# Kernel tuning notes

Hardware: AMD Instinct MI355X
Metric: run time of the kernel (lower is better)

Reference implementation:

```python
import jax, jax.numpy as jnp
import numpy as np
from jax import lax

# ---- Haar (db1) wavelet filters, matching create_wavelet_filter ----
_S2 = float(1.0 / np.sqrt(2.0))
_dec_lo = np.array([_S2, _S2], np.float32)    # pywt dec_lo reversed (symmetric)
_dec_hi = np.array([_S2, -_S2], np.float32)   # pywt dec_hi [-s,s] reversed
_rec_lo = np.array([_S2, _S2], np.float32)    # pywt rec_lo flipped (symmetric)
_rec_hi = np.array([-_S2, _S2], np.float32)   # pywt rec_hi [s,-s] flipped

def _outer(a, b):  # torch: a.unsqueeze(0) * b.unsqueeze(1) -> [i,j] = a[j]*b[i]
    return b[:, None] * a[None, :]

DEC = jnp.asarray(np.stack([_outer(_dec_lo, _dec_lo), _outer(_dec_lo, _dec_hi),
                            _outer(_dec_hi, _dec_lo), _outer(_dec_hi, _dec_hi)]))  # [4,2,2]
REC = jnp.asarray(np.stack([_outer(_rec_lo, _rec_lo), _outer(_rec_lo, _rec_hi),
                            _outer(_rec_hi, _rec_lo), _outer(_rec_hi, _rec_hi)]))  # [4,2,2]

BN_EPS = 1e-5

def mish(x):
    return x * jnp.tanh(jax.nn.softplus(x))

def silu(x):
    return x * jax.nn.sigmoid(x)

def bn(x, g, b):  # eval-mode BatchNorm2d with running_mean=0, running_var=1
    return x * (g / jnp.sqrt(1.0 + BN_EPS))[None, :, None, None] + b[None, :, None, None]

def dwconv(x, w, pad):  # depthwise conv, w: [C,1,k,k]
    return lax.conv_general_dilated(x, w, (1, 1), [(pad, pad), (pad, pad)],
                                    feature_group_count=x.shape[1],
                                    dimension_numbers=('NCHW', 'OIHW', 'NCHW'))

def dyn_dwconv(x, ew, gw):
    # DynamicConv2d (depthwise experts). ew: [E,C,1,k,k], gw: [E,C]
    gates = jax.nn.softmax(x.mean((2, 3)) @ gw.T, axis=-1)  # [B,E]
    k = ew.shape[-1]
    outs = jnp.stack([dwconv(x, ew[e], k // 2) for e in range(ew.shape[0])], 1)  # [B,E,C,H,W]
    return jnp.einsum('be,bechw->bchw', gates, outs)

def local_branch(x, ew, gw, bn1g, bn1b, pw, bn2g, bn2b):
    # DWConv2d_BN_ReLU: dynamic dwconv -> BN -> Mish -> depthwise 1x1 (per-channel scale) -> BN
    y = mish(bn(dyn_dwconv(x, ew, gw), bn1g, bn1b))
    y = y * pw[None, :, None, None]
    return bn(y, bn2g, bn2b)

def sel_scan(u, xw, dtw, dtb, Alog, Dp):
    # u: [B,L,D]; xw: [R+2N,D]; dtw: [D,R]; dtb: [D]; Alog: [D,N]; Dp: [D]
    R = dtw.shape[1]
    N = Alog.shape[1]
    xdbl = jnp.einsum('bld,ed->ble', u, xw)
    dt, Bm, Cm = xdbl[..., :R], xdbl[..., R:R + N], xdbl[..., R + N:]
    delta = jax.nn.softplus(jnp.einsum('blr,dr->bld', dt, dtw) + dtb)  # [B,L,D]
    A = -jnp.exp(Alog)                                                  # [D,N]
    a = jnp.exp(delta[..., None] * A)                                   # [B,L,D,N]
    b = delta[..., None] * Bm[:, :, None, :] * u[..., None]             # [B,L,D,N]
    def comb(c1, c2):
        a1, b1 = c1
        a2, b2 = c2
        return a1 * a2, a2 * b1 + b2
    _, h = lax.associative_scan(comb, (a, b), axis=1)                    # h_t = a_t h_{t-1} + b_t
    return jnp.einsum('bldn,bln->bld', h, Cm) + Dp * u

def ss2d(x, in_w, cw, cb, xpw, dtw, dtb, Alog, Dp, ow):
    # SS2D (d_state=1, k_group=2, channel_first): in_proj -> dwconv+silu -> 2-direction
    # selective scan -> gate with silu(z) -> out_proj.
    B, C, H, W = x.shape
    xz = jnp.einsum('oc,bchw->bohw', in_w, x)
    d = in_w.shape[0] // 2
    xi, z = xz[:, :d], xz[:, d:]
    xc = silu(dwconv(xi, cw, 1) + cb[None, :, None, None])
    u0 = xc.reshape(B, d, H * W).transpose(0, 2, 1)                       # row-major scan
    u1 = xc.transpose(0, 1, 3, 2).reshape(B, d, H * W).transpose(0, 2, 1)  # col-major scan
    y0 = sel_scan(u0, xpw[0], dtw[0], dtb[0], Alog[0], Dp[0])
    y1 = sel_scan(u1, xpw[1], dtw[1], dtb[1], Alog[1], Dp[1])
    y0 = y0.transpose(0, 2, 1).reshape(B, d, H, W)
    y1 = y1.transpose(0, 2, 1).reshape(B, d, W, H).transpose(0, 1, 3, 2)
    y = (y0 + y1) * silu(z)
    return jnp.einsum('oc,bchw->bohw', ow, y)

def mbwt(x, wav_w, wav_b, wav_scale, base_scale,
         ss_in_w, ss_conv_w, ss_conv_b, ss_xproj_w, ss_dt_w, ss_dt_b, ss_A_log, ss_D, ss_out_w):
    # MBWTConv2d, wt_levels=1, H/W even. Haar WT (2x2 stride 2) == block reshape + einsum.
    B, C, H, W = x.shape
    xr = x.reshape(B, C, H // 2, 2, W // 2, 2)
    wt = jnp.einsum('bchpwq,kpq->bckhw', xr, DEC)                  # [B,C,4,h,w]
    tag = wt.reshape(B, 4 * C, H // 2, W // 2)
    tag = dwconv(tag, wav_w, wav_w.shape[-1] // 2) + wav_b[None, :, None, None]
    tag = (tag * wav_scale).reshape(B, C, 4, H // 2, W // 2)
    # inverse Haar WT (conv_transpose 2x2 stride 2, groups=C)
    up = jnp.einsum('bckhw,kpq->bchpwq', tag, REC).reshape(B, C, H, W)
    g = ss2d(x, ss_in_w, ss_conv_w, ss_conv_b, ss_xproj_w, ss_dt_w, ss_dt_b, ss_A_log, ss_D, ss_out_w)
    return base_scale * g + up


def setup_inputs() -> dict:
    key = jax.random.key(0)
    ks = iter(jax.random.split(key, 64))
    B, DIM, H, W = 16, 256, 64, 64
    Cg = Cl = 64
    d = {'x': jax.random.normal(next(ks), (B, DIM, H, W), jnp.float32)}
    for j, k in enumerate((3, 5, 7)):
        p = f'l{j}_'
        d[p + 'ew'] = jax.random.normal(next(ks), (4, Cl, 1, k, k), jnp.float32) * 0.1
        d[p + 'gw'] = jax.random.normal(next(ks), (4, Cl), jnp.float32) * 0.1
        d[p + 'bn1g'] = jnp.ones((Cl,), jnp.float32)
        d[p + 'bn1b'] = jnp.zeros((Cl,), jnp.float32)
        d[p + 'pw'] = jax.random.normal(next(ks), (Cl,), jnp.float32) * 0.2
        d[p + 'bn2g'] = jnp.ones((Cl,), jnp.float32)
        d[p + 'bn2b'] = jnp.zeros((Cl,), jnp.float32)
    d['wav_w'] = jax.random.normal(next(ks), (4 * Cg, 1, 3, 3), jnp.float32) * 0.1
    d['wav_b'] = jnp.zeros((4 * Cg,), jnp.float32)
    d['wav_scale'] = jnp.full((1, 4 * Cg, 1, 1), 0.1, jnp.float32)
    d['base_scale'] = jnp.ones((1, Cg, 1, 1), jnp.float32)
    dm, R, N, K = Cg, 4, 1, 2  # d_inner, dt_rank, d_state, k_group
    d['ss_in_w'] = jax.random.normal(next(ks), (2 * dm, Cg), jnp.float32) * float(1 / np.sqrt(Cg))
    d['ss_conv_w'] = jax.random.normal(next(ks), (dm, 1, 3, 3), jnp.float32) * 0.1
    d['ss_conv_b'] = jnp.zeros((dm,), jnp.float32)
    d['ss_xproj_w'] = jax.random.normal(next(ks), (K, R + 2 * N, dm), jnp.float32) * float(1 / np.sqrt(dm))
    d['ss_dt_w'] = jax.random.normal(next(ks), (K, dm, R), jnp.float32) * float(1 / np.sqrt(R))
    d['ss_dt_b'] = jnp.full((K, dm), -2.0, jnp.float32)
    d['ss_A_log'] = jnp.zeros((K, dm, N), jnp.float32)
    d['ss_D'] = jnp.ones((K, dm), jnp.float32)
    d['ss_out_w'] = jax.random.normal(next(ks), (Cg, dm), jnp.float32) * float(1 / np.sqrt(dm))
    return d


def reference(x,
              l0_ew, l0_gw, l0_bn1g, l0_bn1b, l0_pw, l0_bn2g, l0_bn2b,
              l1_ew, l1_gw, l1_bn1g, l1_bn1b, l1_pw, l1_bn2g, l1_bn2b,
              l2_ew, l2_gw, l2_bn1g, l2_bn1b, l2_pw, l2_bn2g, l2_bn2b,
              wav_w, wav_b, wav_scale, base_scale,
              ss_in_w, ss_conv_w, ss_conv_b, ss_xproj_w, ss_dt_w, ss_dt_b, ss_A_log, ss_D, ss_out_w):
    Cg, Cl = 64, 64
    xg, xl, xi = x[:, :Cg], x[:, Cg:Cg + Cl], x[:, Cg + Cl:]
    yl = (local_branch(xl, l0_ew, l0_gw, l0_bn1g, l0_bn1b, l0_pw, l0_bn2g, l0_bn2b)
          + local_branch(xl, l1_ew, l1_gw, l1_bn1g, l1_bn1b, l1_pw, l1_bn2g, l1_bn2b)
          + local_branch(xl, l2_ew, l2_gw, l2_bn1g, l2_bn1b, l2_pw, l2_bn2g, l2_bn2b))
    yg = mbwt(xg, wav_w, wav_b, wav_scale, base_scale,
              ss_in_w, ss_conv_w, ss_conv_b, ss_xproj_w, ss_dt_w, ss_dt_b, ss_A_log, ss_D, ss_out_w)
    return jnp.concatenate([yg, yl, xi], axis=1)
```

## Files before the change

### kernel.cpp

```cpp
#include <hip/hip_runtime.h>
#include <math.h>

static constexpr int NB   = 16;
static constexpr int DIM  = 256;
static constexpr int CG   = 64;
static constexpr int HH   = 64;
static constexpr int WW   = 64;
static constexpr int HW   = HH * WW;

__device__ __forceinline__ float mish_fast(float x) {
    float t = __expf(fminf(x, 20.f));
    float p = __builtin_fmaf(t, t, t + t);
    return x * p * __builtin_amdgcn_rcpf(p + 2.f);
}
__device__ __forceinline__ float silu_f(float x) {
    return x * __builtin_amdgcn_rcpf(1.f + __expf(-x));
}
__device__ __forceinline__ float softplus_fast(float x) {
    return fmaxf(x, 0.f) + __logf(1.f + __expf(-fabsf(x)));
}

__global__ __launch_bounds__(256) void k_stage1(
    const float* __restrict__ x,
    const float* __restrict__ wav_w, const float* __restrict__ wav_b,
    const float* __restrict__ wav_scale,
    float* __restrict__ up, float* __restrict__ mean,
    const float* __restrict__ in_w,
    float* __restrict__ xi, float* __restrict__ z,
    float* __restrict__ out) {
    __shared__ float smem[4608];
    int bid = blockIdx.x;
    int tid = threadIdx.x;
    int role = bid % 7;

    if (role < 4) {
        int aid = (bid / 7) * 4 + role;
        int c = aid & 63, b = aid >> 6;
        float* wtb = smem;
        float* red = smem + 4352;
        const float* xp = x + ((size_t)b * DIM + c) * HW;

        {
            const float4* lp4 = (const float4*)(x + ((size_t)b * DIM + 64 + c) * HW);
            float s = 0.f;
            for (int i = tid; i < 1024; i += 256) {
                float4 v = lp4[i];
                s += (v.x + v.y) + (v.z + v.w);
            }
            red[tid] = s;
            __syncthreads();
            for (int o = 128; o > 0; o >>= 1) {
                if (tid < o) red[tid] += red[tid + o];
                __syncthreads();
            }
            if (tid == 0) mean[b * 64 + c] = red[0] * (1.f / HW);
        }

#pragma unroll
        for (int it = 0; it < 2; ++it) {
            int p = tid + it * 256;
            int h = p >> 4, w2 = p & 15;
            float4 top = *(const float4*)(xp + (2 * h) * 64 + 4 * w2);
            float4 bot = *(const float4*)(xp + (2 * h + 1) * 64 + 4 * w2);
            float a0 = top.x, b0 = top.y, c0q = bot.x, d0 = bot.y;
            float a1 = top.z, b1 = top.w, c1q = bot.z, d1 = bot.w;
            int base0 = h * 34 + 2 * w2;
            *(float2*)(wtb + 0 * 1088 + base0) =
                make_float2(0.5f * (a0 + b0 + c0q + d0), 0.5f * (a1 + b1 + c1q + d1));
            *(float2*)(wtb + 1 * 1088 + base0) =
                make_float2(0.5f * (a0 + b0 - c0q - d0), 0.5f * (a1 + b1 - c1q - d1));
            *(float2*)(wtb + 2 * 1088 + base0) =
                make_float2(0.5f * (a0 - b0 + c0q - d0), 0.5f * (a1 - b1 + c1q - d1));
            *(float2*)(wtb + 3 * 1088 + base0) =
                make_float2(0.5f * (a0 - b0 - c0q + d0), 0.5f * (a1 - b1 - c1q + d1));
        }
        __syncthreads();

        float wk[4][9], tb[4];
#pragma unroll
        for (int k = 0; k < 4; ++k) {
            int ch = c * 4 + k;
            float sc = wav_scale[ch];
#pragma unroll
            for (int j = 0; j < 9; ++j) wk[k][j] = wav_w[ch * 9 + j] * sc;
            tb[k] = wav_b[ch] * sc;
        }
        float* upp = up + ((size_t)b * CG + c) * HW;
        for (int i = tid; i < 1024; i += 256) {
            int h = i >> 5, w = i & 31;
            float tg[4];
#pragma unroll
            for (int k = 0; k < 4; ++k) {
                float s = tb[k];
#pragma unroll
                for (int dy = -1; dy <= 1; ++dy) {
                    int hh = h + dy;
                    if (hh < 0 || hh >= 32) continue;
#pragma unroll
                    for (int dx = -1; dx <= 1; ++dx) {
                        int wx = w + dx;
                        if (wx < 0 || wx >= 32) continue;
                        s = fmaf(wtb[k * 1088 + hh * 34 + wx], wk[k][(dy + 1) * 3 + (dx + 1)], s);
                    }
                }
                tg[k] = s;
            }
            float u00 = 0.5f * (tg[0] - tg[1] - tg[2] + tg[3]);
            float u01 = 0.5f * (tg[0] - tg[1] + tg[2] - tg[3]);
            float u10 = 0.5f * (tg[0] + tg[1] - tg[2] - tg[3]);
            float u11 = 0.5f * (tg[0] + tg[1] + tg[2] + tg[3]);
            *(float2*)(upp + (2 * h) * 64 + 2 * w)     = make_float2(u00, u01);
            *(float2*)(upp + (2 * h + 1) * 64 + 2 * w) = make_float2(u10, u11);
        }
    } else if (role < 6) {
        int did = (bid / 7) * 2 + (role - 4);
        int h0 = (did & 31) * 2;
        int b  = did >> 5;
        float* xs = smem;
        float* wt = smem + 2048;

        float acc[8][8];
#pragma unroll
        for (int i = 0; i < 8; ++i)
#pragma unroll
            for (int j = 0; j < 8; ++j) acc[i][j] = 0.f;

        int o0 = (tid >> 4) * 8;
        int p0 = (tid & 15) * 8;

        for (int ko = 0; ko < 64; ko += 16) {
            if (ko) __syncthreads();
            {
                int s = tid;
#pragma unroll
                for (int it = 0; it < 2; ++it, s += 256) {
                    int c = s >> 5, p4 = (s & 31) * 4;
                    float4 v = *(const float4*)(x + ((size_t)b * DIM + ko + c) * HW + h0 * 64 + p4);
                    *(float4*)(xs + c * 128 + p4) = v;
                }
            }
            {
                int s = tid;
#pragma unroll
                for (int it = 0; it < 2; ++it, s += 256) {
                    int o = s >> 2, c0 = (s & 3) * 4;
                    float4 v = *(const float4*)(in_w + o * 64 + ko + c0);
#pragma unroll
                    for (int i = 0; i < 4; ++i) {
                        int cc = c0 + i;
                        int osw = o ^ (((cc >> 2) & 3) << 3);
                        wt[cc * 128 + osw] = ((const float*)&v)[i];
                    }
                }
            }
            __syncthreads();
#pragma unroll 4
            for (int c = 0; c < 16; ++c) {
                int osw = o0 ^ (((c >> 2) & 3) << 3);
                float xv[8], wv[8];
                *(float4*)(xv)     = *(const float4*)(xs + c * 128 + p0);
                *(float4*)(xv + 4) = *(const float4*)(xs + c * 128 + p0 + 4);
                *(float4*)(wv)     = *(const float4*)(wt + c * 128 + osw);
                *(float4*)(wv + 4) = *(const float4*)(wt + c * 128 + osw + 4);
#pragma unroll
                for (int i = 0; i < 8; ++i)
#pragma unroll
                    for (int j = 0; j < 8; ++j)
                        acc[i][j] = fmaf(wv[i], xv[j], acc[i][j]);
            }
        }

#pragma unroll
        for (int i = 0; i < 8; ++i) {
            int o = o0 + i;
            float* dst = (o < 64) ? (xi + ((size_t)b * 64 + o) * HW + h0 * 64)
                                  : (z + ((size_t)b * 64 + (o - 64)) * HW + h0 * 64);
            *(float4*)(dst + p0)     = make_float4(acc[i][0], acc[i][1], acc[i][2], acc[i][3]);
            *(float4*)(dst + p0 + 4) = make_float4(acc[i][4], acc[i][5], acc[i][6], acc[i][7]);
        }
    } else {
        int pid = bid / 7;
        const float4* x4 = (const float4*)x;
        float4* o4 = (float4*)out;
        int base = pid * 8192;
#pragma unroll
        for (int it = 0; it < 32; ++it) {
            int idx = base + it * 256 + tid;
            int bb = idx >> 17;
            int r  = idx & 131071;
            int gi = bb * 262144 + 131072 + r;
            o4[gi] = x4[gi];
        }
    }
}

__global__ __launch_bounds__(256) void k_stage2(
    const float* __restrict__ xi,
    const float* __restrict__ cw, const float* __restrict__ cb,
    const float* __restrict__ xpw,
    float* __restrict__ xc, float4* __restrict__ proj4, float2* __restrict__ projBC,
    const float* __restrict__ mean,
    const float* __restrict__ ew3, const float* __restrict__ gw3, const float* __restrict__ g13,
    const float* __restrict__ ew5, const float* __restrict__ gw5, const float* __restrict__ g15,
    const float* __restrict__ ew7, const float* __restrict__ gw7, const float* __restrict__ g17,
    float* __restrict__ w3o, float* __restrict__ w5o, float* __restrict__ w7o) {
    __shared__ float smem[6304];
    int bid = blockIdx.x;
    int tid = threadIdx.x;

    if (bid < 512) {
        int h0 = (bid & 31) * 2;
        int b  = bid >> 5;
        float* xs  = smem;
        float* xcs = smem + 4224;

        int dir = tid >> 7;
        int px  = tid & 127;
        float acc0 = 0.f, acc1 = 0.f, acc2 = 0.f, acc3 = 0.f, acc4 = 0.f, acc5 = 0.f;

        int cl_c = tid >> 4;
        int p0_c = (tid & 15) * 8;
        int row_c = p0_c >> 6;
        int wb_c  = p0_c & 63;

        for (int ch0 = 0; ch0 < 64; ch0 += 16) {
            if (ch0) __syncthreads();
            {
                int s = tid;
#pragma unroll
                for (int it = 0; it < 4; ++it, s += 256) {
                    int c = s >> 6;
                    int rem = s & 63;
                    int r = rem >> 4, w4 = (rem & 15) * 4;
                    int gh = h0 - 1 + r;
                    float4 v = make_float4(0.f, 0.f, 0.f, 0.f);
                    if (gh >= 0 && gh < 64)
                        v = *(const float4*)(xi + ((size_t)b * 64 + ch0 + c) * HW + gh * 64 + w4);
                    float* dp = xs + c * 264 + r * 66 + 1 + w4;
                    dp[0] = v.x; dp[1] = v.y; dp[2] = v.z; dp[3] = v.w;
                }
                if (tid < 64) {
                    int cl = tid >> 2, r = tid & 3;
                    xs[cl * 264 + r * 66 + 0]  = 0.f;
                    xs[cl * 264 + r * 66 + 65] = 0.f;
                }
            }
            __syncthreads();

            {
                float wk[9];
#pragma unroll
                for (int j = 0; j < 9; ++j) wk[j] = cw[(ch0 + cl_c) * 9 + j];
                float bias = cb[ch0 + cl_c];
                float accr[8];
#pragma unroll
                for (int k = 0; k < 8; ++k) accr[k] = bias;
#pragma unroll
                for (int dy = 0; dy < 3; ++dy) {
                    const float* rp = xs + cl_c * 264 + (row_c + dy) * 66 + wb_c;
                    float r[10];
#pragma unroll
                    for (int q = 0; q < 10; ++q) r[q] = rp[q];
#pragma unroll
                    for (int k = 0; k < 8; ++k)
#pragma unroll
                        for (int dx = 0; dx < 3; ++dx)
                            accr[k] = fmaf(r[k + dx], wk[dy * 3 + dx], accr[k]);
                }
#pragma unroll
                for (int k = 0; k < 8; ++k)
                    xcs[cl_c * 130 + p0_c + k] = silu_f(accr[k]);
            }
            __syncthreads();

            {
                int s = tid;
#pragma unroll
                for (int it = 0; it < 2; ++it, s += 256) {
                    int c = s >> 5, pq = (s & 31) * 4;
                    const float* sp = xcs + c * 130 + pq;
                    *(float4*)(xc + ((size_t)b * 64 + ch0 + c) * HW + h0 * 64 + pq) =
                        make_float4(sp[0], sp[1], sp[2], sp[3]);
                }
            }
            {
                const float* wp = xpw + dir * 6 * 64 + ch0;
#pragma unroll 8
                for (int c = 0; c < 16; ++c) {
                    float xv = xcs[c * 130 + px];
                    acc0 = fmaf(xv, wp[0 * 64 + c], acc0);
                    acc1 = fmaf(xv, wp[1 * 64 + c], acc1);
                    acc2 = fmaf(xv, wp[2 * 64 + c], acc2);
                    acc3 = fmaf(xv, wp[3 * 64 + c], acc3);
                    acc4 = fmaf(xv, wp[4 * 64 + c], acc4);
                    acc5 = fmaf(xv, wp[5 * 64 + c], acc5);
                }
            }
        }

        int h = h0 + (px >> 6), w = px & 63;
        int l = (dir == 0) ? (h * 64 + w) : (w * 64 + h);
        size_t base = ((size_t)dir * NB + b) * HW + l;
        proj4[base]  = make_float4(acc0, acc1, acc2, acc3);
        projBC[base] = make_float2(acc4, acc5);
    } else {
        int b = bid - 512;
        int c = tid;
        float* m = smem;
        float* g = smem + 64;
        if (c < 64) m[c] = mean[b * 64 + c];
        __syncthreads();
        const float rs = rsqrtf(1.f + 1e-5f);

#define WEFF_SECT(GW, EW, G1, OUT, K2)                                        \
        {                                                                     \
            if (c < 4) {                                                      \
                float l = 0.f;                                                \
                for (int cc = 0; cc < 64; ++cc) l += m[cc] * GW[c * 64 + cc]; \
                g[c] = l;                                                     \
            }                                                                 \
            __syncthreads();                                                  \
            if (c == 0) {                                                     \
                float mx = fmaxf(fmaxf(g[0], g[1]), fmaxf(g[2], g[3]));       \
                float e0 = expf(g[0] - mx), e1 = expf(g[1] - mx);             \
                float e2 = expf(g[2] - mx), e3 = expf(g[3] - mx);             \
                float inv = 1.f / (e0 + e1 + e2 + e3);                        \
                g[0] = e0 * inv; g[1] = e1 * inv; g[2] = e2 * inv; g[3] = e3 * inv; \
            }                                                                 \
            __syncthreads();                                                  \
            if (c < 64) {                                                     \
                float g1s = G1[c] * rs;                                       \
                for (int kk = 0; kk < K2; ++kk) {                             \
                    float w = 0.f;                                            \
                    for (int e = 0; e < 4; ++e) w += g[e] * EW[(e * 64 + c) * K2 + kk]; \
                    OUT[(b * 64 + c) * K2 + kk] = w * g1s;                    \
                }                                                             \
            }                                                                 \
            __syncthreads();                                                  \
        }

        WEFF_SECT(gw3, ew3, g13, w3o, 9)
        WEFF_SECT(gw5, ew5, g15, w5o, 25)
        WEFF_SECT(gw7, ew7, g17, w7o, 49)
#undef WEFF_SECT
    }
}

__global__ __launch_bounds__(256) void k_scan2(const float* __restrict__ xc,
                                               const float4* __restrict__ proj4,
                                               const float2* __restrict__ projBC,
                                               const float* __restrict__ dt_w,
                                               const float* __restrict__ dt_b,
                                               const float* __restrict__ A_log,
                                               const float* __restrict__ Dp,
                                               const float* __restrict__ z,
                                               float* __restrict__ yz) {
    int wave = threadIdx.x >> 6;
    int lane = threadIdx.x & 63;
    int wid = blockIdx.x;
    int b = wid >> 6;
    int d = wid & 63;

    __shared__ float ut[64 * 65];
    __shared__ float al[4][1088];
    __shared__ float bl[4][1088];
    __shared__ float aggA[4], aggB[4];

    const float* uplane = xc + ((size_t)b * 64 + d) * HW;
    const float4* up4 = (const float4*)uplane;
#pragma unroll
    for (int q = 0; q < 4; ++q) {
        int s = q * 256 + threadIdx.x;
        float4 v = up4[s];
        int r = s >> 4, c0 = (s & 15) * 4;
        float* p = ut + r * 65 + c0;
        p[0] = v.x; p[1] = v.y; p[2] = v.z; p[3] = v.w;
    }
    __syncthreads();

    int ch = wave;
    float* a_my = al[wave];
    float* b_my = bl[wave];
    float y0r[16];

    {
        float4 wv = *(const float4*)(dt_w + d * 4);
        float db = dt_b[d];
        float A = -__expf(A_log[d]);
        float Dv = Dp[d];
        const float4* p4 = proj4 + (size_t)b * HW;
        const float2* pBC = projBC + (size_t)b * HW;

        float uv[16], cm[16];
#pragma unroll
        for (int j = 0; j < 16; ++j) {
            int el = j * 64 + lane;
            int e  = ch * 1024 + el;
            float4 t4 = p4[e];
            float2 t2 = pBC[e];
            float u = ut[(ch * 16 + j) * 65 + lane];
            uv[j] = u; cm[j] = t2.y;
            float pre = fmaf(t4.x, wv.x, fmaf(t4.y, wv.y,
                        fmaf(t4.z, wv.z, fmaf(t4.w, wv.w, db))));
            float delta = softplus_fast(pre);
            float aj = __expf(delta * A);
            float bj = delta * t2.x * u;
            int idx = (el >> 4) * 17 + (el & 15);
            a_my[idx] = aj;
            b_my[idx] = bj;
        }
        __builtin_amdgcn_wave_barrier();

        float a[16], bb[16];
#pragma unroll
        for (int j = 0; j < 16; ++j) {
            a[j]  = a_my[lane * 17 + j];
            bb[j] = b_my[lane * 17 + j];
        }
        float As = 1.f, Bs = 0.f;
#pragma unroll
        for (int j = 0; j < 16; ++j) { Bs = fmaf(a[j], Bs, bb[j]); As *= a[j]; }
        float Ai = As, Bi = Bs;
#pragma unroll
        for (int off = 1; off < 64; off <<= 1) {
            float ap = __shfl_up(Ai, (unsigned)off, 64);
            float bp = __shfl_up(Bi, (unsigned)off, 64);
            if (lane >= off) { Bi = fmaf(Ai, bp, Bi); Ai *= ap; }
        }
        if (lane == 63) { aggA[wave] = Ai; aggB[wave] = Bi; }
        __syncthreads();
        float carry = 0.f;
        for (int k = 0; k < wave; ++k) carry = fmaf(aggA[k], carry, aggB[k]);
        float ap1 = __shfl_up(Ai, 1, 64);
        float bp1 = __shfl_up(Bi, 1, 64);
        float h = (lane == 0) ? carry : fmaf(ap1, carry, bp1);
#pragma unroll
        for (int j = 0; j < 16; ++j) {
            h = fmaf(a[j], h, bb[j]);
            a_my[lane * 17 + j] = h;
        }
        __builtin_amdgcn_wave_barrier();
#pragma unroll
        for (int j = 0; j < 16; ++j) {
            int el = j * 64 + lane;
            float hv = a_my[(el >> 4) * 17 + (el & 15)];
            y0r[j] = fmaf(hv, cm[j], Dv * uv[j]);
        }
    }
    __syncthreads();

    {
        int pd = 64 + d;
        float4 wv = *(const float4*)(dt_w + pd * 4);
        float db = dt_b[pd];
        float A = -__expf(A_log[pd]);
        float Dv = Dp[pd];
        const float4* p4 = proj4 + ((size_t)NB + b) * HW;
        const float2* pBC = projBC + ((size_t)NB + b) * HW;

        float uv[16], cm[16];
#pragma unroll
        for (int j = 0; j < 16; ++j) {
            int el = j * 64 + lane;
            int e  = ch * 1024 + el;
            float4 t4 = p4[e];
            float2 t2 = pBC[e];
            float u = ut[lane * 65 + (ch * 16 + j)];
            uv[j] = u; cm[j] = t2.y;
            float pre = fmaf(t4.x, wv.x, fmaf(t4.y, wv.y,
                        fmaf(t4.z, wv.z, fmaf(t4.w, wv.w, db))));
            float delta = softplus_fast(pre);
            float aj = __expf(delta * A);
            float bj = delta * t2.x * u;
            int idx = (el >> 4) * 17 + (el & 15);
            a_my[idx] = aj;
            b_my[idx] = bj;
        }
        __builtin_amdgcn_wave_barrier();

        float a[16], bb[16];
#pragma unroll
        for (int j = 0; j < 16; ++j) {
            a[j]  = a_my[lane * 17 + j];
            bb[j] = b_my[lane * 17 + j];
        }
        float As = 1.f, Bs = 0.f;
#pragma unroll
        for (int j = 0; j < 16; ++j) { Bs = fmaf(a[j], Bs, bb[j]); As *= a[j]; }
        float Ai = As, Bi = Bs;
#pragma unroll
        for (int off = 1; off < 64; off <<= 1) {
            float ap = __shfl_up(Ai, (unsigned)off, 64);
            float bp = __shfl_up(Bi, (unsigned)off, 64);
            if (lane >= off) { Bi = fmaf(Ai, bp, Bi); Ai *= ap; }
        }
        if (lane == 63) { aggA[wave] = Ai; aggB[wave] = Bi; }
        __syncthreads();
        float carry = 0.f;
        for (int k = 0; k < wave; ++k) carry = fmaf(aggA[k], carry, aggB[k]);
        float ap1 = __shfl_up(Ai, 1, 64);
        float bp1 = __shfl_up(Bi, 1, 64);
        float h = (lane == 0) ? carry : fmaf(ap1, carry, bp1);
#pragma unroll
        for (int j = 0; j < 16; ++j) {
            h = fmaf(a[j], h, bb[j]);
            a_my[lane * 17 + j] = h;
        }
        __builtin_amdgcn_wave_barrier();
#pragma unroll
        for (int j = 0; j < 16; ++j) {
            int el = j * 64 + lane;
            float hv = a_my[(el >> 4) * 17 + (el & 15)];
            ut[lane * 65 + (ch * 16 + j)] = fmaf(hv, cm[j], Dv * uv[j]);
        }
    }
    __syncthreads();

    const float* zp = z + ((size_t)b * 64 + d) * HW;
    float* yp = yz + ((size_t)b * 64 + d) * HW;
#pragma unroll
    for (int j = 0; j < 16; ++j) {
        int e = ch * 1024 + j * 64 + lane;
        float y1v = ut[(ch * 16 + j) * 65 + lane];
        float zz = zp[e];
        yp[e] = (y0r[j] + y1v) * silu_f(zz);
    }
}

__global__ __launch_bounds__(256) void k_stage4(
    const float* __restrict__ x,
    const float* __restrict__ w3, const float* __restrict__ w5, const float* __restrict__ w7,
    const float* __restrict__ b1_0, const float* __restrict__ pw0,
    const float* __restrict__ g2_0, const float* __restrict__ b2_0,
    const float* __restrict__ b1_1, const float* __restrict__ pw1,
    const float* __restrict__ g2_1, const float* __restrict__ b2_1,
    const float* __restrict__ b1_2, const float* __restrict__ pw2,
    const float* __restrict__ g2_2, const float* __restrict__ b2_2,
    const float* __restrict__ yz, const float* __restrict__ ow,
    const float* __restrict__ base_scale, const float* __restrict__ up,
    float* __restrict__ out) {
    __shared__ float smem[3072];
    int bid = blockIdx.x;
    int tid = threadIdx.x;

    if (bid % 9 != 8) {
        int cidx = (bid / 9) * 8 + (bid % 9);
        int tile = cidx & 3;
        int c = (cidx >> 2) & 63;
        int b = cidx >> 8;
        int oy = (tile >> 1) * 32, ox = (tile & 1) * 32;
        float* t = smem;
        const float* xp = x + ((size_t)b * DIM + 64 + c) * HW;
        for (int i = tid; i < 38 * 38; i += 256) {
            int r = i / 38, cc = i % 38;
            int yy = r - 3 + oy, xx = cc - 3 + ox;
            t[r * 40 + cc] = (yy >= 0 && yy < 64 && xx >= 0 && xx < 64) ? xp[yy * 64 + xx] : 0.f;
        }
        const float* w3p = w3 + (b * 64 + c) * 9;
        const float* w5p = w5 + (b * 64 + c) * 25;
        const float* w7p = w7 + (b * 64 + c) * 49;
        float W3r[9], W5r[25], W7r[49];
#pragma unroll
        for (int j = 0; j < 9; ++j)  W3r[j] = w3p[j];
#pragma unroll
        for (int j = 0; j < 25; ++j) W5r[j] = w5p[j];
#pragma unroll
        for (int j = 0; j < 49; ++j) W7r[j] = w7p[j];
        __syncthreads();

        const float rs = rsqrtf(1.f + 1e-5f);
        float bb1a = b1_0[c], bb1b = b1_1[c], bb1c = b1_2[c];
        float ssa = pw0[c] * g2_0[c] * rs, ssb = pw1[c] * g2_1[c] * rs, ssc = pw2[c] * g2_2[c] * rs;
        float bb2a = b2_0[c], bb2b = b2_1[c], bb2c = b2_2[c];

        int y  = tid >> 3;
        int x0 = (tid & 7) * 4;

        float a3[4] = {0.f, 0.f, 0.f, 0.f};
        float a5[4] = {0.f, 0.f, 0.f, 0.f};
        float a7[4] = {0.f, 0.f, 0.f, 0.f};

#pragma unroll
        for (int dy = 0; dy < 7; ++dy) {
            const float4* rp = (const float4*)(t + (y + dy) * 40 + x0);
            float4 q0 = rp[0], q1 = rp[1], q2 = rp[2];
            float r[12] = {q0.x, q0.y, q0.z, q0.w, q1.x, q1.y, q1.z, q1.w,
                           q2.x, q2.y, q2.z, q2.w};
#pragma unroll
            for (int k = 0; k < 4; ++k)
#pragma unroll
                for (int dx = 0; dx < 7; ++dx)
                    a7[k] = fmaf(r[k + dx], W7r[dy * 7 + dx], a7[k]);
            if (dy >= 1 && dy <= 5) {
                int ey = dy - 1;
#pragma unroll
                for (int k = 0; k < 4; ++k)
#pragma unroll
                    for (int dx = 0; dx < 5; ++dx)
                        a5[k] = fmaf(r[k + 1 + dx], W5r[ey * 5 + dx], a5[k]);
            }
            if (dy >= 2 && dy <= 4) {
                int ey = dy - 2;
#pragma unroll
                for (int k = 0; k < 4; ++k)
#pragma unroll
                    for (int dx = 0; dx < 3; ++dx)
                        a3[k] = fmaf(r[k + 2 + dx], W3r[ey * 3 + dx], a3[k]);
            }
        }

        float4 res;
        float* rr = (float*)&res;
#pragma unroll
        for (int k = 0; k < 4; ++k) {
            rr[k] = mish_fast(a3[k] + bb1a) * ssa + bb2a
                  + mish_fast(a5[k] + bb1b) * ssb + bb2b
                  + mish_fast(a7[k] + bb1c) * ssc + bb2c;
        }
        float* op = out + ((size_t)b * DIM + 64 + c) * HW;
        *(float4*)(op + (oy + y) * 64 + ox + x0) = res;
    } else {
        int id2 = bid / 9;
        int h0 = (id2 & 31) * 2;
        int b  = id2 >> 5;
        float* yv = smem;
        float* wt = smem + 2048;

        float acc[8][4];
#pragma unroll
        for (int i = 0; i < 8; ++i)
#pragma unroll
            for (int j = 0; j < 4; ++j) acc[i][j] = 0.f;

        int o0 = (tid >> 5) * 8;
        int p0 = (tid & 31) * 4;

        for (int ko = 0; ko < 64; ko += 16) {
            if (ko) __syncthreads();
            {
                int s = tid;
#pragma unroll
                for (int it = 0; it < 2; ++it, s += 256) {
                    int c = s >> 5, p4 = (s & 31) * 4;
                    size_t idx = ((size_t)b * 64 + ko + c) * HW + h0 * 64 + p4;
                    *(float4*)(yv + c * 128 + p4) = *(const float4*)(yz + idx);
                }
            }
            {
                int o = tid >> 2, c0 = (tid & 3) * 4;
                float4 v = *(const float4*)(ow + o * 64 + ko + c0);
#pragma unroll
                for (int i = 0; i < 4; ++i) {
                    int cc = c0 + i;
                    int osw = o ^ (((cc >> 2) & 3) << 3);
                    wt[cc * 64 + osw] = ((const float*)&v)[i];
                }
            }
            __syncthreads();
#pragma unroll 4
            for (int c = 0; c < 16; ++c) {
                int osw = o0 ^ (((c >> 2) & 3) << 3);
                float wv[8], xv[4];
                *(float4*)(wv)     = *(const float4*)(wt + c * 64 + osw);
                *(float4*)(wv + 4) = *(const float4*)(wt + c * 64 + osw + 4);
                *(float4*)(xv)     = *(const float4*)(yv + c * 128 + p0);
#pragma unroll
                for (int i = 0; i < 8; ++i)
#pragma unroll
                    for (int j = 0; j < 4; ++j)
                        acc[i][j] = fmaf(wv[i], xv[j], acc[i][j]);
            }
        }

#pragma unroll
        for (int i = 0; i < 8; ++i) {
            int o = o0 + i;
            float bs = base_scale[o];
            float4 u = *(const float4*)(up + ((size_t)b * 64 + o) * HW + h0 * 64 + p0);
            float4 r = make_float4(fmaf(bs, acc[i][0], u.x),
                                   fmaf(bs, acc[i][1], u.y),
                                   fmaf(bs, acc[i][2], u.z),
                                   fmaf(bs, acc[i][3], u.w));
            *(float4*)(out + ((size_t)b * DIM + o) * HW + h0 * 64 + p0) = r;
        }
    }
}

extern "C" void kernel_launch(void* const* d_in, const int* in_sizes, int n_in,
                              void* d_out, int out_size, void* d_ws, size_t ws_size,
                              hipStream_t stream) {
    (void)in_sizes; (void)n_in; (void)out_size; (void)ws_size;
    const float* x = (const float*)d_in[0];
    float* out = (float*)d_out;
    float* ws = (float*)d_ws;

    const size_t IMG = (size_t)NB * 64 * HW;
    float* buf_xi   = ws;
    float* buf_z    = ws + IMG;
    float* buf_xc   = ws + 2 * IMG;
    float* buf_up   = ws + 3 * IMG;
    float* buf_p4   = ws + 4 * IMG;
    float* buf_pBC  = buf_p4 + (size_t)4 * 2 * NB * HW;
    float* buf_mean = buf_pBC + (size_t)2 * 2 * NB * HW;
    float* buf_w3   = buf_mean + 1024;
    float* buf_w5   = buf_w3 + 16 * 64 * 9;
    float* buf_w7   = buf_w5 + 16 * 64 * 25;

    k_stage1<<<1792, 256, 0, stream>>>(x,
        (const float*)d_in[22], (const float*)d_in[23], (const float*)d_in[24],
        buf_up, buf_mean,
        (const float*)d_in[26], buf_xi, buf_z, out);

    k_stage2<<<528, 256, 0, stream>>>(buf_xi,
        (const float*)d_in[27], (const float*)d_in[28], (const float*)d_in[29],
        buf_xc, (float4*)buf_p4, (float2*)buf_pBC,
        buf_mean,
        (const float*)d_in[1],  (const float*)d_in[2],  (const float*)d_in[3],
        (const float*)d_in[8],  (const float*)d_in[9],  (const float*)d_in[10],
        (const float*)d_in[15], (const float*)d_in[16], (const float*)d_in[17],
        buf_w3, buf_w5, buf_w7);

    k_scan2<<<1024, 256, 0, stream>>>(buf_xc, (const float4*)buf_p4, (const float2*)buf_pBC,
        (const float*)d_in[30], (const float*)d_in[31],
        (const float*)d_in[32], (const float*)d_in[33],
        buf_z, buf_xi);

    k_stage4<<<4608, 256, 0, stream>>>(x, buf_w3, buf_w5, buf_w7,
        (const float*)d_in[4],  (const float*)d_in[5],  (const float*)d_in[6],  (const float*)d_in[7],
        (const float*)d_in[11], (const float*)d_in[12], (const float*)d_in[13], (const float*)d_in[14],
        (const float*)d_in[18], (const float*)d_in[19], (const float*)d_in[20], (const float*)d_in[21],
        buf_xi, (const float*)d_in[34], (const float*)d_in[25], buf_up, out);
}
```

Before: 120.2 us.

## Move passthrough copy from stage1 into stage4 blocks and prefetch wavelet inputs

Removes the dedicated passthrough-copy blocks from stage1, shrinking its grid, and spreads the copy of the untouched channels into the conv-role blocks of stage4, where each block copies a small slice. It also issues the Haar input loads before the mean reduction so their latency overlaps the reduction. The aim is to balance work across kernels and hide memory latency. In exchange, stage4 blocks carry extra global traffic, and each thread in stage1 holds more registers for the early loads.

After: 120.2 us. No clear change (+0.0%).

```diff
diff --git a/kernel.cpp b/kernel.cpp
--- a/kernel.cpp
+++ b/kernel.cpp
@@ -26,19 +26,25 @@
     const float* __restrict__ wav_scale,
     float* __restrict__ up, float* __restrict__ mean,
     const float* __restrict__ in_w,
-    float* __restrict__ xi, float* __restrict__ z,
-    float* __restrict__ out) {
+    float* __restrict__ xi, float* __restrict__ z) {
     __shared__ float smem[4608];
     int bid = blockIdx.x;
     int tid = threadIdx.x;
-    int role = bid % 7;
-
-    if (role < 4) {
-        int aid = (bid / 7) * 4 + role;
+
+    if (bid % 3 != 2) {
+        int aid = (bid / 3) * 2 + (bid % 3);
         int c = aid & 63, b = aid >> 6;
         float* wtb = smem;
         float* red = smem + 4352;
         const float* xp = x + ((size_t)b * DIM + c) * HW;
+
+        int p0h = tid, p1h = tid + 256;
+        int h0h = p0h >> 4, w20 = p0h & 15;
+        int h1h = p1h >> 4, w21 = p1h & 15;
+        float4 top0 = *(const float4*)(xp + (2 * h0h) * 64 + 4 * w20);
+        float4 bot0 = *(const float4*)(xp + (2 * h0h + 1) * 64 + 4 * w20);
+        float4 top1 = *(const float4*)(xp + (2 * h1h) * 64 + 4 * w21);
+        float4 bot1 = *(const float4*)(xp + (2 * h1h + 1) * 64 + 4 * w21);
 
         {
             const float4* lp4 = (const float4*)(x + ((size_t)b * DIM + 64 + c) * HW);
@@ -56,15 +62,10 @@
             if (tid == 0) mean[b * 64 + c] = red[0] * (1.f / HW);
         }
 
-#pragma unroll
-        for (int it = 0; it < 2; ++it) {
-            int p = tid + it * 256;
-            int h = p >> 4, w2 = p & 15;
-            float4 top = *(const float4*)(xp + (2 * h) * 64 + 4 * w2);
-            float4 bot = *(const float4*)(xp + (2 * h + 1) * 64 + 4 * w2);
-            float a0 = top.x, b0 = top.y, c0q = bot.x, d0 = bot.y;
-            float a1 = top.z, b1 = top.w, c1q = bot.z, d1 = bot.w;
-            int base0 = h * 34 + 2 * w2;
+        {
+            float a0 = top0.x, b0 = top0.y, c0q = bot0.x, d0 = bot0.y;
+            float a1 = top0.z, b1 = top0.w, c1q = bot0.z, d1 = bot0.w;
+            int base0 = h0h * 34 + 2 * w20;
             *(float2*)(wtb + 0 * 1088 + base0) =
                 make_float2(0.5f * (a0 + b0 + c0q + d0), 0.5f * (a1 + b1 + c1q + d1));
             *(float2*)(wtb + 1 * 1088 + base0) =
@@ -73,6 +74,17 @@
                 make_float2(0.5f * (a0 - b0 + c0q - d0), 0.5f * (a1 - b1 + c1q - d1));
             *(float2*)(wtb + 3 * 1088 + base0) =
                 make_float2(0.5f * (a0 - b0 - c0q + d0), 0.5f * (a1 - b1 - c1q + d1));
+            a0 = top1.x; b0 = top1.y; c0q = bot1.x; d0 = bot1.y;
+            a1 = top1.z; b1 = top1.w; c1q = bot1.z; d1 = bot1.w;
+            int base1 = h1h * 34 + 2 * w21;
+            *(float2*)(wtb + 0 * 1088 + base1) =
+                make_float2(0.5f * (a0 + b0 + c0q + d0), 0.5f * (a1 + b1 + c1q + d1));
+            *(float2*)(wtb + 1 * 1088 + base1) =
+                make_float2(0.5f * (a0 + b0 - c0q - d0), 0.5f * (a1 + b1 - c1q - d1));
+            *(float2*)(wtb + 2 * 1088 + base1) =
+                make_float2(0.5f * (a0 - b0 + c0q - d0), 0.5f * (a1 - b1 + c1q - d1));
+            *(float2*)(wtb + 3 * 1088 + base1) =
+                make_float2(0.5f * (a0 - b0 - c0q + d0), 0.5f * (a1 - b1 - c1q + d1));
         }
         __syncthreads();
 
@@ -112,8 +124,8 @@
             *(float2*)(upp + (2 * h) * 64 + 2 * w)     = make_float2(u00, u01);
             *(float2*)(upp + (2 * h + 1) * 64 + 2 * w) = make_float2(u10, u11);
         }
-    } else if (role < 6) {
-        int did = (bid / 7) * 2 + (role - 4);
+    } else {
+        int did = bid / 3;
         int h0 = (did & 31) * 2;
         int b  = did >> 5;
         float* xs = smem;
@@ -177,19 +189,6 @@
                                   : (z + ((size_t)b * 64 + (o - 64)) * HW + h0 * 64);
             *(float4*)(dst + p0)     = make_float4(acc[i][0], acc[i][1], acc[i][2], acc[i][3]);
             *(float4*)(dst + p0 + 4) = make_float4(acc[i][4], acc[i][5], acc[i][6], acc[i][7]);
-        }
-    } else {
-        int pid = bid / 7;
-        const float4* x4 = (const float4*)x;
-        float4* o4 = (float4*)out;
-        int base = pid * 8192;
-#pragma unroll
-        for (int it = 0; it < 32; ++it) {
-            int idx = base + it * 256 + tid;
-            int bb = idx >> 17;
-            int r  = idx & 131071;
-            int gi = bb * 262144 + 131072 + r;
-            o4[gi] = x4[gi];
         }
     }
 }
@@ -556,6 +555,19 @@
             int yy = r - 3 + oy, xx = cc - 3 + ox;
             t[r * 40 + cc] = (yy >= 0 && yy < 64 && xx >= 0 && xx < 64) ? xp[yy * 64 + xx] : 0.f;
         }
+        {
+            const float4* x4 = (const float4*)x;
+            float4* o4 = (float4*)out;
+            int base = cidx * 512;
+#pragma unroll
+            for (int it = 0; it < 2; ++it) {
+                int idx = base + it * 256 + tid;
+                int bb = idx >> 17;
+                int r  = idx & 131071;
+                int gi = bb * 262144 + 131072 + r;
+                o4[gi] = x4[gi];
+            }
+        }
         const float* w3p = w3 + (b * 64 + c) * 9;
         const float* w5p = w5 + (b * 64 + c) * 25;
         const float* w7p = w7 + (b * 64 + c) * 49;
@@ -706,10 +718,10 @@
     float* buf_w5   = buf_w3 + 16 * 64 * 9;
     float* buf_w7   = buf_w5 + 16 * 64 * 25;
 
-    k_stage1<<<1792, 256, 0, stream>>>(x,
+    k_stage1<<<1536, 256, 0, stream>>>(x,
         (const float*)d_in[22], (const float*)d_in[23], (const float*)d_in[24],
         buf_up, buf_mean,
-        (const float*)d_in[26], buf_xi, buf_z, out);
+        (const float*)d_in[26], buf_xi, buf_z);
 
     k_stage2<<<528, 256, 0, stream>>>(buf_xi,
         (const float*)d_in[27], (const float*)d_in[28], (const float*)d_in[29],
```
